# Kernel optimization log

Measured on AMD Instinct MI355X. Metric: run time of the kernel, lower is better.

## Reference

```python
import jax, jax.numpy as jnp
import numpy as np

EPS = 1e-8

def setup_inputs() -> dict:
    key = jax.random.key(0)
    k1, k2, k3, k4 = jax.random.split(key, 4)
    x_cnn = jax.random.normal(k1, (8, 256, 128, 128), dtype=jnp.float32)
    x_vit = jax.random.normal(k2, (8, 512, 32, 32), dtype=jnp.float32)
    W = jax.random.normal(k3, (256, 512), dtype=jnp.float32) * 0.05  # 1x1 conv weight
    b = jax.random.normal(k4, (256,), dtype=jnp.float32) * 0.05
    return {"x_cnn": x_cnn, "x_vit": x_vit, "W": W, "b": b}

def reference(x_cnn, x_vit, W, b):
    # 1x1 conv projection: 512 -> cnn_channels
    v = jnp.einsum('oc,bchw->bohw', W, x_vit) + b[None, :, None, None]
    B, C, H, Wd = x_cnn.shape
    if v.shape[2:] != (H, Wd):
        # bilinear, half-pixel centers == torch align_corners=False
        v = jax.image.resize(v, (B, C, H, Wd), method='bilinear')
    # Per-pixel cosine similarity over channels. The original computes a full
    # (HW x HW) bmm and keeps only the diagonal; the diagonal equals this
    # per-pixel channel dot product, so the math is identical.
    dot = jnp.sum(x_cnn * v, axis=1)               # [B,H,W]
    n_cnn = jnp.sqrt(jnp.sum(x_cnn * x_cnn, axis=1))
    n_vit = jnp.sqrt(jnp.sum(v * v, axis=1))
    sim = dot / (n_cnn * n_vit + EPS)
    return sim[:, None, :, :]                      # [B,1,H,W]
```

## Files before the change

kernel.cpp:

```cpp
#include <hip/hip_runtime.h>
#include <hip/hip_bf16.h>

typedef __attribute__((ext_vector_type(8))) short bf16x8;
typedef __attribute__((ext_vector_type(4))) float f32x4;
typedef __attribute__((ext_vector_type(8))) unsigned short u16x8;
typedef __attribute__((ext_vector_type(4), aligned(4))) float f32x4u;

static __device__ __forceinline__ unsigned short f2bf(float f) {
    union { float f; unsigned int u; } v; v.f = f;
    unsigned int u = v.u;
    u += 0x7FFFu + ((u >> 16) & 1u);
    return (unsigned short)(u >> 16);
}

__global__ void __launch_bounds__(256) convert_w(const float* __restrict__ W,
                                                 unsigned short* __restrict__ Wbf) {
    int i = (blockIdx.x * 256 + threadIdx.x) * 4;
    float4 v = *(const float4*)(W + i);
    ushort4 o;
    o.x = f2bf(v.x); o.y = f2bf(v.y); o.z = f2bf(v.z); o.w = f2bf(v.w);
    *(ushort4*)(Wbf + i) = o;
}

__global__ void __launch_bounds__(256) transpose_xvit(const float* __restrict__ X,
                                                      unsigned short* __restrict__ Xt) {
    __shared__ unsigned short ls[64][65];
    int b  = blockIdx.z;
    int c0 = blockIdx.y * 64;
    int p0 = blockIdx.x * 64;
    int t  = threadIdx.x;

    const float* src = X + ((size_t)b * 512 + c0) * 1024 + p0;
    int cc = t >> 4;
    int p4 = (t & 15) << 2;
    #pragma unroll
    for (int i = 0; i < 4; ++i) {
        int c = cc + i * 16;
        float4 v = *(const float4*)(src + (size_t)c * 1024 + p4);
        ls[p4 + 0][c] = f2bf(v.x);
        ls[p4 + 1][c] = f2bf(v.y);
        ls[p4 + 2][c] = f2bf(v.z);
        ls[p4 + 3][c] = f2bf(v.w);
    }
    __syncthreads();

    unsigned short* dst = Xt + ((size_t)b * 1024 + p0) * 512 + c0;
    int pp  = t >> 2;
    int c16 = (t & 3) << 4;
    u16x8 w0, w1;
    #pragma unroll
    for (int j = 0; j < 8; ++j) { w0[j] = ls[pp][c16 + j]; w1[j] = ls[pp][c16 + 8 + j]; }
    *(u16x8*)(dst + (size_t)pp * 512 + c16)     = w0;
    *(u16x8*)(dst + (size_t)pp * 512 + c16 + 8) = w1;
}

__global__ void __launch_bounds__(256) gemm_bf16(const unsigned short* __restrict__ Wbf,
                                                 const unsigned short* __restrict__ Xt,
                                                 const float* __restrict__ bias,
                                                 float* __restrict__ V) {
    __shared__ __align__(16) unsigned short As[64 * 32];
    __shared__ __align__(16) unsigned short Bs[64 * 32];

    int b  = blockIdx.z;
    int m0 = blockIdx.y * 64;
    int n0 = blockIdx.x * 64;
    int t  = threadIdx.x;
    int wave = t >> 6;
    int lane = t & 63;
    int wm = (wave >> 1) * 32;
    int wn = (wave & 1) * 32;
    int l15  = lane & 15;
    int quad = lane >> 4;

    const unsigned short* Aglob = Wbf + (size_t)(m0 + (t >> 2)) * 512 + ((t & 3) << 3);
    const unsigned short* Bglob = Xt + ((size_t)b * 1024 + n0 + (t >> 2)) * 512 + ((t & 3) << 3);
    unsigned short* Asw = As + (t >> 2) * 32 + ((t & 3) << 3);
    unsigned short* Bsw = Bs + (t >> 2) * 32 + ((t & 3) << 3);

    f32x4 acc[2][2] = {};

    for (int k0 = 0; k0 < 512; k0 += 32) {
        *(u16x8*)Asw = *(const u16x8*)(Aglob + k0);
        *(u16x8*)Bsw = *(const u16x8*)(Bglob + k0);
        __syncthreads();

        bf16x8 a0 = *(const bf16x8*)(As + (wm + l15) * 32 + quad * 8);
        bf16x8 a1 = *(const bf16x8*)(As + (wm + 16 + l15) * 32 + quad * 8);
        bf16x8 b0 = *(const bf16x8*)(Bs + (wn + l15) * 32 + quad * 8);
        bf16x8 b1 = *(const bf16x8*)(Bs + (wn + 16 + l15) * 32 + quad * 8);

        acc[0][0] = __builtin_amdgcn_mfma_f32_16x16x32_bf16(a0, b0, acc[0][0], 0, 0, 0);
        acc[0][1] = __builtin_amdgcn_mfma_f32_16x16x32_bf16(a0, b1, acc[0][1], 0, 0, 0);
        acc[1][0] = __builtin_amdgcn_mfma_f32_16x16x32_bf16(a1, b0, acc[1][0], 0, 0, 0);
        acc[1][1] = __builtin_amdgcn_mfma_f32_16x16x32_bf16(a1, b1, acc[1][1], 0, 0, 0);
        __syncthreads();
    }

    #pragma unroll
    for (int mi = 0; mi < 2; ++mi)
        #pragma unroll
        for (int ni = 0; ni < 2; ++ni)
            #pragma unroll
            for (int r = 0; r < 4; ++r) {
                int gm = m0 + wm + mi * 16 + quad * 4 + r;
                int gn = n0 + wn + ni * 16 + l15;
                V[((size_t)b * 256 + gm) * 1024 + gn] = acc[mi][ni][r] + bias[gm];
            }
}

__global__ void __launch_bounds__(256) fused_cos(const float* __restrict__ xcnn,
                                                 const float* __restrict__ V,
                                                 float* __restrict__ out) {
    __shared__ float red[8 * 385];

    int bh = blockIdx.x;
    int b  = bh >> 7;
    int h  = bh & 127;
    int t  = threadIdx.x;
    int q  = t & 31;
    int cs = t >> 5;

    float sy = (h + 0.5f) * 0.25f - 0.5f;
    float fy = floorf(sy);
    float dy = sy - fy;
    int y0 = max(0, min(31, (int)fy));
    int y1 = max(0, min(31, (int)fy + 1));

    int cb = max(0, min(28, q - 1));
    float a[4][4];
    #pragma unroll
    for (int px = 0; px < 4; ++px) {
        #pragma unroll
        for (int j = 0; j < 4; ++j) a[px][j] = 0.f;
        int w = q * 4 + px;
        float sx = (w + 0.5f) * 0.25f - 0.5f;
        float fx = floorf(sx);
        float dx = sx - fx;
        int x0 = max(0, min(31, (int)fx));
        int x1 = max(0, min(31, (int)fx + 1));
        a[px][x0 - cb] += 1.f - dx;
        a[px][x1 - cb] += dx;
    }

    const float* xp = xcnn + ((size_t)(b * 256 + cs * 32) * 16384) + h * 128 + q * 4;
    const float* vt = V + ((size_t)(b * 256 + cs * 32) * 1024) + y0 * 32 + cb;
    const float* vb = V + ((size_t)(b * 256 + cs * 32) * 1024) + y1 * 32 + cb;
    float ry = dy, ry0 = 1.f - dy;

    float dot[4] = {0.f, 0.f, 0.f, 0.f};
    float nx [4] = {0.f, 0.f, 0.f, 0.f};
    float nv [4] = {0.f, 0.f, 0.f, 0.f};

    #pragma unroll 8
    for (int c = 0; c < 32; ++c) {
        float4  xv  = *(const float4*)(xp + (size_t)c * 16384);
        f32x4u  top = *(const f32x4u*)(vt + (size_t)c * 1024);
        f32x4u  bot = *(const f32x4u*)(vb + (size_t)c * 1024);
        float bl0 = ry0 * top[0] + ry * bot[0];
        float bl1 = ry0 * top[1] + ry * bot[1];
        float bl2 = ry0 * top[2] + ry * bot[2];
        float bl3 = ry0 * top[3] + ry * bot[3];
        float xs[4] = {xv.x, xv.y, xv.z, xv.w};
        #pragma unroll
        for (int px = 0; px < 4; ++px) {
            float v = a[px][0] * bl0 + a[px][1] * bl1 + a[px][2] * bl2 + a[px][3] * bl3;
            dot[px] += xs[px] * v;
            nx [px] += xs[px] * xs[px];
            nv [px] += v * v;
        }
    }

    float* my = red + cs * 385;
    #pragma unroll
    for (int px = 0; px < 4; ++px) {
        int o = (q * 4 + px) * 3;
        my[o + 0] = dot[px];
        my[o + 1] = nx[px];
        my[o + 2] = nv[px];
    }
    __syncthreads();

    if (t < 128) {
        int px = t & 3;
        int q2 = t >> 2;
        int o  = (q2 * 4 + px) * 3;
        float d = 0.f, sx2 = 0.f, sv2 = 0.f;
        #pragma unroll
        for (int s = 0; s < 8; ++s) {
            d   += red[s * 385 + o + 0];
            sx2 += red[s * 385 + o + 1];
            sv2 += red[s * 385 + o + 2];
        }
        out[(size_t)b * 16384 + h * 128 + q2 * 4 + px] =
            d / (sqrtf(sx2) * sqrtf(sv2) + 1e-8f);
    }
}

extern "C" void kernel_launch(void* const* d_in, const int* in_sizes, int n_in,
                              void* d_out, int out_size, void* d_ws, size_t ws_size,
                              hipStream_t stream) {
    const float* x_cnn = (const float*)d_in[0];
    const float* x_vit = (const float*)d_in[1];
    const float* W     = (const float*)d_in[2];
    const float* bias  = (const float*)d_in[3];
    float* out = (float*)d_out;

    char* ws = (char*)d_ws;
    float*          V   = (float*)ws;
    unsigned short* Xt  = (unsigned short*)(ws + 8388608);
    unsigned short* Wbf = (unsigned short*)(ws + 16777216);

    convert_w<<<128, 256, 0, stream>>>(W, Wbf);
    transpose_xvit<<<dim3(16, 8, 8), 256, 0, stream>>>(x_vit, Xt);
    gemm_bf16<<<dim3(16, 4, 8), 256, 0, stream>>>(Wbf, Xt, bias, V);
    fused_cos<<<1024, 256, 0, stream>>>(x_cnn, V, out);
}
```

Measured before the change: 223.1 us.

## Fuse bf16 conversion and x_vit transpose into GEMM tile loads

Removes the separate weight-conversion and x_vit transpose kernels. The GEMM now reads fp32 W and x_vit directly, converts to bf16 in registers, and writes B transposed into padded shared memory (stride 40). This drops two launches and the round trip through a bf16 workspace. In exchange, the GEMM issues more global traffic per tile (fp32 loads, W reloaded by every block) and does scattered 2-byte LDS stores for B.

New measurement: 224.3 us. Within noise of the previous version (+0.5%).

```diff
diff --git a/kernel.cpp b/kernel.cpp
--- a/kernel.cpp
+++ b/kernel.cpp
@@ -13,53 +13,13 @@
     return (unsigned short)(u >> 16);
 }
 
-__global__ void __launch_bounds__(256) convert_w(const float* __restrict__ W,
-                                                 unsigned short* __restrict__ Wbf) {
-    int i = (blockIdx.x * 256 + threadIdx.x) * 4;
-    float4 v = *(const float4*)(W + i);
-    ushort4 o;
-    o.x = f2bf(v.x); o.y = f2bf(v.y); o.z = f2bf(v.z); o.w = f2bf(v.w);
-    *(ushort4*)(Wbf + i) = o;
-}
-
-__global__ void __launch_bounds__(256) transpose_xvit(const float* __restrict__ X,
-                                                      unsigned short* __restrict__ Xt) {
-    __shared__ unsigned short ls[64][65];
-    int b  = blockIdx.z;
-    int c0 = blockIdx.y * 64;
-    int p0 = blockIdx.x * 64;
-    int t  = threadIdx.x;
-
-    const float* src = X + ((size_t)b * 512 + c0) * 1024 + p0;
-    int cc = t >> 4;
-    int p4 = (t & 15) << 2;
-    #pragma unroll
-    for (int i = 0; i < 4; ++i) {
-        int c = cc + i * 16;
-        float4 v = *(const float4*)(src + (size_t)c * 1024 + p4);
-        ls[p4 + 0][c] = f2bf(v.x);
-        ls[p4 + 1][c] = f2bf(v.y);
-        ls[p4 + 2][c] = f2bf(v.z);
-        ls[p4 + 3][c] = f2bf(v.w);
-    }
-    __syncthreads();
-
-    unsigned short* dst = Xt + ((size_t)b * 1024 + p0) * 512 + c0;
-    int pp  = t >> 2;
-    int c16 = (t & 3) << 4;
-    u16x8 w0, w1;
-    #pragma unroll
-    for (int j = 0; j < 8; ++j) { w0[j] = ls[pp][c16 + j]; w1[j] = ls[pp][c16 + 8 + j]; }
-    *(u16x8*)(dst + (size_t)pp * 512 + c16)     = w0;
-    *(u16x8*)(dst + (size_t)pp * 512 + c16 + 8) = w1;
-}
-
-__global__ void __launch_bounds__(256) gemm_bf16(const unsigned short* __restrict__ Wbf,
-                                                 const unsigned short* __restrict__ Xt,
-                                                 const float* __restrict__ bias,
-                                                 float* __restrict__ V) {
-    __shared__ __align__(16) unsigned short As[64 * 32];
-    __shared__ __align__(16) unsigned short Bs[64 * 32];
+#define TS 40
+__global__ void __launch_bounds__(256) gemm_fused(const float* __restrict__ W,
+                                                  const float* __restrict__ Xv,
+                                                  const float* __restrict__ bias,
+                                                  float* __restrict__ V) {
+    __shared__ __align__(16) unsigned short As[64 * TS];
+    __shared__ __align__(16) unsigned short Bs[64 * TS];
 
     int b  = blockIdx.z;
     int m0 = blockIdx.y * 64;
@@ -72,22 +32,38 @@
     int l15  = lane & 15;
     int quad = lane >> 4;
 
-    const unsigned short* Aglob = Wbf + (size_t)(m0 + (t >> 2)) * 512 + ((t & 3) << 3);
-    const unsigned short* Bglob = Xt + ((size_t)b * 1024 + n0 + (t >> 2)) * 512 + ((t & 3) << 3);
-    unsigned short* Asw = As + (t >> 2) * 32 + ((t & 3) << 3);
-    unsigned short* Bsw = Bs + (t >> 2) * 32 + ((t & 3) << 3);
+    const float* Ag = W + (size_t)(m0 + (t >> 2)) * 512 + ((t & 3) << 3);
+    unsigned short* Asw = As + (t >> 2) * TS + ((t & 3) << 3);
+    const float* Bg = Xv + ((size_t)b * 512 + (t >> 3)) * 1024 + n0 + ((t & 7) << 3);
+    int bs_n = (t & 7) << 3;
+    int bs_k = t >> 3;
 
     f32x4 acc[2][2] = {};
 
     for (int k0 = 0; k0 < 512; k0 += 32) {
-        *(u16x8*)Asw = *(const u16x8*)(Aglob + k0);
-        *(u16x8*)Bsw = *(const u16x8*)(Bglob + k0);
+        float4 av0 = *(const float4*)(Ag + k0);
+        float4 av1 = *(const float4*)(Ag + k0 + 4);
+        float4 bv0 = *(const float4*)(Bg + (size_t)k0 * 1024);
+        float4 bv1 = *(const float4*)(Bg + (size_t)k0 * 1024 + 4);
+
+        u16x8 aw;
+        aw[0] = f2bf(av0.x); aw[1] = f2bf(av0.y); aw[2] = f2bf(av0.z); aw[3] = f2bf(av0.w);
+        aw[4] = f2bf(av1.x); aw[5] = f2bf(av1.y); aw[6] = f2bf(av1.z); aw[7] = f2bf(av1.w);
+        *(u16x8*)Asw = aw;
+
+        unsigned short bw[8];
+        bw[0] = f2bf(bv0.x); bw[1] = f2bf(bv0.y); bw[2] = f2bf(bv0.z); bw[3] = f2bf(bv0.w);
+        bw[4] = f2bf(bv1.x); bw[5] = f2bf(bv1.y); bw[6] = f2bf(bv1.z); bw[7] = f2bf(bv1.w);
+        #pragma unroll
+        for (int j = 0; j < 8; ++j)
+            Bs[(bs_n + j) * TS + bs_k] = bw[j];
+
         __syncthreads();
 
-        bf16x8 a0 = *(const bf16x8*)(As + (wm + l15) * 32 + quad * 8);
-        bf16x8 a1 = *(const bf16x8*)(As + (wm + 16 + l15) * 32 + quad * 8);
-        bf16x8 b0 = *(const bf16x8*)(Bs + (wn + l15) * 32 + quad * 8);
-        bf16x8 b1 = *(const bf16x8*)(Bs + (wn + 16 + l15) * 32 + quad * 8);
+        bf16x8 a0 = *(const bf16x8*)(As + (wm + l15) * TS + quad * 8);
+        bf16x8 a1 = *(const bf16x8*)(As + (wm + 16 + l15) * TS + quad * 8);
+        bf16x8 b0 = *(const bf16x8*)(Bs + (wn + l15) * TS + quad * 8);
+        bf16x8 b1 = *(const bf16x8*)(Bs + (wn + 16 + l15) * TS + quad * 8);
 
         acc[0][0] = __builtin_amdgcn_mfma_f32_16x16x32_bf16(a0, b0, acc[0][0], 0, 0, 0);
         acc[0][1] = __builtin_amdgcn_mfma_f32_16x16x32_bf16(a0, b1, acc[0][1], 0, 0, 0);
@@ -205,13 +181,8 @@
     const float* bias  = (const float*)d_in[3];
     float* out = (float*)d_out;
 
-    char* ws = (char*)d_ws;
-    float*          V   = (float*)ws;
-    unsigned short* Xt  = (unsigned short*)(ws + 8388608);
-    unsigned short* Wbf = (unsigned short*)(ws + 16777216);
+    float* V = (float*)d_ws;
 
-    convert_w<<<128, 256, 0, stream>>>(W, Wbf);
-    transpose_xvit<<<dim3(16, 8, 8), 256, 0, stream>>>(x_vit, Xt);
-    gemm_bf16<<<dim3(16, 4, 8), 256, 0, stream>>>(Wbf, Xt, bias, V);
+    gemm_fused<<<dim3(16, 4, 8), 256, 0, stream>>>(W, x_vit, bias, V);
     fused_cos<<<1024, 256, 0, stream>>>(x_cnn, V, out);
 }
```
